# Kernel tuning notes

Measured on AMD Instinct MI355X. Metric: run time of the kernel, lower is better.

## Reference

```python
import jax, jax.numpy as jnp
import numpy as np

INTRA_K = 16
OUTER_K = 16
MAX_PAIR = 1024


def _mahalanobis(x, cov_inv, mean):
    # x: (..., D) difference vectors; returns squared Mahalanobis-style form (...,)
    xc = x - mean
    return jnp.einsum('...i,ij,...j->...', xc, cov_inv, xc)


def setup_inputs() -> dict:
    key = jax.random.key(0)
    k1, k2, k3 = jax.random.split(key, 3)
    B, N, M = 4, 1024, 1024
    outputs = jax.random.normal(k1, (B, N, 9), dtype=jnp.float32)
    targets = jax.random.normal(k2, (B, M, 9), dtype=jnp.float32)
    mask = jax.random.randint(k3, (B, M), 0, 2).astype(bool)
    return {"outputs": outputs, "targets": targets, "mask": mask}


def reference(outputs, targets, mask):
    y_pred = outputs[:, :MAX_PAIR]                      # (B, N, 9)
    m = mask.astype(y_pred.dtype)                       # (B, M)
    cnt = m.sum()

    # mean / covariance over masked true grasps (equivalent to boolean-gather)
    mean = (targets * m[..., None]).sum((0, 1)) / cnt   # (9,)
    centered = (targets - mean) * m[..., None]          # masked rows contribute 0
    flat = centered.reshape(-1, 9)
    cov = flat.T @ flat / (cnt - 1.0)                   # (9, 9)
    cov_inv = jnp.linalg.pinv(cov)

    # intra loss: true-vs-pred pairwise distances, masked rows excluded
    diff = targets[:, :, None, :] - y_pred[:, None, :, :]   # (B, M, N, 9)
    d = _mahalanobis(diff, cov_inv, mean)                   # (B, M, N)
    neg_topk, _ = jax.lax.top_k(-d, INTRA_K)                # k smallest
    row_sum = (-neg_topk).sum(-1)                           # (B, M)
    intra_loss = (row_sum * m).sum() / cnt                  # mean over masked rows

    # outer loss: pred-vs-pred pairwise distances, no mask
    diff_r = y_pred[:, None, :, :] - y_pred[:, :, None, :]  # (B, N, N, 9); [b,i,j] = pred[b,j]-pred[b,i]
    d_r = _mahalanobis(diff_r, cov_inv, mean)               # (B, N, N)
    neg_tk, _ = jax.lax.top_k(-d_r, OUTER_K)
    outer_loss = (-neg_tk).mean()

    return intra_loss, intra_loss, outer_loss
```

## Files before the change

### kernel.cpp

```cpp
#include <hip/hip_runtime.h>
#include <math.h>

#define BB    4
#define MM    1024
#define NN    1024
#define DD    9
#define KSEL  16
#define NROW  (BB * MM)
#define NBLKD (NROW / 4)

struct Ws {
  float yT[BB * DD * NN];
  float qy[BB * NN];
  float bpart_i[NBLKD];
  float bpart_o[NBLKD];
  float part[16][55];
  float cnt;
  float mean[DD];
  float cinv[DD * DD];
  unsigned ticket;
};

__global__ __launch_bounds__(256) void stats_kernel(
    const float* __restrict__ targets, const int* __restrict__ mask,
    Ws* __restrict__ ws) {
  const int tid = threadIdx.x;
  const int r = blockIdx.x * 256 + tid;
  if (blockIdx.x == 0 && tid == 0) ws->ticket = 0u;

  float acc[55];
#pragma unroll
  for (int k = 0; k < 55; ++k) acc[k] = 0.f;
  if (mask[r] != 0) {
    float t[DD];
#pragma unroll
    for (int k = 0; k < DD; ++k) t[k] = targets[r * DD + k];
    acc[0] = 1.f;
#pragma unroll
    for (int k = 0; k < DD; ++k) acc[1 + k] = t[k];
    int u = 10;
#pragma unroll
    for (int p = 0; p < DD; ++p)
#pragma unroll
      for (int q = p; q < DD; ++q) acc[u++] = t[p] * t[q];
  }

  __shared__ float lds[4][55];
#pragma unroll
  for (int k = 0; k < 55; ++k) {
    float v = acc[k];
#pragma unroll
    for (int off = 32; off > 0; off >>= 1) v += __shfl_down(v, off, 64);
    if ((tid & 63) == 0) lds[tid >> 6][k] = v;
  }
  __syncthreads();
  if (tid < 55)
    ws->part[blockIdx.x][tid] =
        lds[0][tid] + lds[1][tid] + lds[2][tid] + lds[3][tid];
}

__global__ __launch_bounds__(256) void prep_kernel(
    const float* __restrict__ outputs, Ws* __restrict__ ws) {
  const int tid = threadIdx.x;
  __shared__ double Sd[55];
  __shared__ float Cs[DD * DD];

  if (tid < 55) {
    double s = 0.0;
#pragma unroll
    for (int b = 0; b < 16; ++b) s += (double)ws->part[b][tid];
    Sd[tid] = s;
  }
  __syncthreads();

  if (tid < 64) {
    const double cnt = Sd[0];
    const int p = (tid < DD) ? tid : 0;
    double row[2 * DD];
    {
      const double mu_p = Sd[1 + p] / cnt;
#pragma unroll
      for (int q = 0; q < DD; ++q) {
        const int pp = (p < q) ? p : q;
        const int qq = (p < q) ? q : p;
        const int idx = 10 + 9 * pp - (pp * (pp - 1)) / 2 + (qq - pp);
        row[q] = (Sd[idx] - cnt * mu_p * (Sd[1 + q] / cnt)) / (cnt - 1.0);
        row[DD + q] = (p == q) ? 1.0 : 0.0;
      }
    }
#pragma unroll
    for (int c = 0; c < DD; ++c) {
      const double diag = __shfl(row[c], c, 64);
      const double dinv = 1.0 / diag;
      if (tid == c) {
#pragma unroll
        for (int q = 0; q < 2 * DD; ++q) row[q] *= dinv;
      }
      const double f = (tid == c) ? 0.0 : row[c];
#pragma unroll
      for (int q = 0; q < 2 * DD; ++q) {
        const double pv = __shfl(row[q], c, 64);
        row[q] -= f * pv;
      }
    }
    if (tid < DD) {
#pragma unroll
      for (int q = 0; q < DD; ++q) {
        const float cf = (float)row[DD + q];
        Cs[tid * DD + q] = cf;
        if (blockIdx.x == 0) ws->cinv[tid * DD + q] = cf;
      }
    }
    if (tid == 0 && blockIdx.x == 0) {
      ws->cnt = (float)cnt;
#pragma unroll
      for (int q = 0; q < DD; ++q) ws->mean[q] = (float)(Sd[1 + q] / cnt);
    }
  }
  __syncthreads();

  const int j = blockIdx.x * 256 + tid;
  const int b = j >> 10;
  const int jj = j & (NN - 1);
  float y[DD];
#pragma unroll
  for (int k = 0; k < DD; ++k) y[k] = outputs[j * DD + k];
  float q = 0.f;
#pragma unroll
  for (int p = 0; p < DD; ++p) {
    float s = 0.f;
#pragma unroll
    for (int t = 0; t < DD; ++t) s += Cs[p * DD + t] * y[t];
    q += y[p] * s;
    ws->yT[(b * DD + p) * NN + jj] = y[p];
  }
  ws->qy[j] = q;
}

__device__ __forceinline__ float topk16_sum(float v[16]) {
#pragma unroll
  for (int k = 2; k <= 16; k <<= 1) {
#pragma unroll
    for (int j = k >> 1; j > 0; j >>= 1) {
#pragma unroll
      for (int i = 0; i < 16; ++i) {
        const int l = i ^ j;
        if (l > i) {
          const bool up = ((i & k) == 0);
          const float lo = fminf(v[i], v[l]);
          const float hi = fmaxf(v[i], v[l]);
          v[i] = up ? lo : hi;
          v[l] = up ? hi : lo;
        }
      }
    }
  }
#pragma unroll
  for (int off = 1; off < 64; off <<= 1) {
    float pr[16];
#pragma unroll
    for (int i = 0; i < 16; ++i) pr[i] = __shfl_xor(v[i], off, 64);
#pragma unroll
    for (int i = 0; i < 16; ++i) v[i] = fminf(v[i], pr[15 - i]);
    if (off < 32) {
#pragma unroll
      for (int j = 8; j > 0; j >>= 1) {
#pragma unroll
        for (int i = 0; i < 16; ++i) {
          const int l = i ^ j;
          if (l > i) {
            const float lo = fminf(v[i], v[l]);
            const float hi = fmaxf(v[i], v[l]);
            v[i] = lo;
            v[l] = hi;
          }
        }
      }
    }
  }
  float t = v[0];
#pragma unroll
  for (int k = 1; k < 16; ++k) t += v[k];
  return t;
}

__global__ __launch_bounds__(256) void dist_kernel(
    const float* __restrict__ outputs, const float* __restrict__ targets,
    const int* __restrict__ mask, Ws* __restrict__ ws,
    float* __restrict__ out) {
  const int wv = threadIdx.x >> 6;
  const int lane = threadIdx.x & 63;
  const int r = blockIdx.x * 4 + wv;
  const int b = r >> 10;

  float ai[DD], ao[DD];
#pragma unroll
  for (int k = 0; k < DD; ++k) {
    const float m = ws->mean[k];
    ai[k] = targets[r * DD + k] - m;
    ao[k] = outputs[r * DD + k] + m;
  }
  float wi[DD], wo[DD];
  float qai = 0.f, qao = 0.f;
#pragma unroll
  for (int p = 0; p < DD; ++p) {
    float si = 0.f, so = 0.f;
#pragma unroll
    for (int t = 0; t < DD; ++t) {
      const float c = ws->cinv[p * DD + t];
      si += c * ai[t];
      so += c * ao[t];
    }
    wi[p] = si;
    wo[p] = so;
    qai += ai[p] * si;
    qao += ao[p] * so;
  }

  float vi[16], vo[16];
#pragma unroll
  for (int k = 0; k < 16; ++k) { vi[k] = 0.f; vo[k] = 0.f; }
  const float* __restrict__ yTb = ws->yT + (size_t)b * DD * NN;
#pragma unroll
  for (int p = 0; p < DD; ++p) {
    const float4* __restrict__ pl = (const float4*)(yTb + (size_t)p * NN);
    const float wip = wi[p], wop = wo[p];
#pragma unroll
    for (int c = 0; c < 4; ++c) {
      const float4 y4 = pl[c * 64 + lane];
      vi[c * 4 + 0] += wip * y4.x; vo[c * 4 + 0] += wop * y4.x;
      vi[c * 4 + 1] += wip * y4.y; vo[c * 4 + 1] += wop * y4.y;
      vi[c * 4 + 2] += wip * y4.z; vo[c * 4 + 2] += wop * y4.z;
      vi[c * 4 + 3] += wip * y4.w; vo[c * 4 + 3] += wop * y4.w;
    }
  }
  {
    const float4* __restrict__ q4 = (const float4*)(ws->qy + (size_t)b * NN);
#pragma unroll
    for (int c = 0; c < 4; ++c) {
      const float4 qv = q4[c * 64 + lane];
      vi[c * 4 + 0] = qai + qv.x - 2.f * vi[c * 4 + 0];
      vi[c * 4 + 1] = qai + qv.y - 2.f * vi[c * 4 + 1];
      vi[c * 4 + 2] = qai + qv.z - 2.f * vi[c * 4 + 2];
      vi[c * 4 + 3] = qai + qv.w - 2.f * vi[c * 4 + 3];
      vo[c * 4 + 0] = qao + qv.x - 2.f * vo[c * 4 + 0];
      vo[c * 4 + 1] = qao + qv.y - 2.f * vo[c * 4 + 1];
      vo[c * 4 + 2] = qao + qv.z - 2.f * vo[c * 4 + 2];
      vo[c * 4 + 3] = qao + qv.w - 2.f * vo[c * 4 + 3];
    }
  }

  float tot_i = topk16_sum(vi);
  float tot_o = topk16_sum(vo);
  if (mask[r] == 0) tot_i = 0.f;

  __shared__ float s_i[4], s_o[4];
  __shared__ int s_last;
  if (lane == 0) { s_i[wv] = tot_i; s_o[wv] = tot_o; }
  __syncthreads();
  if (threadIdx.x == 0) {
    ws->bpart_i[blockIdx.x] = s_i[0] + s_i[1] + s_i[2] + s_i[3];
    ws->bpart_o[blockIdx.x] = s_o[0] + s_o[1] + s_o[2] + s_o[3];
    __threadfence();
    const unsigned t = atomicAdd(&ws->ticket, 1u);
    s_last = (t == NBLKD - 1) ? 1 : 0;
  }
  __syncthreads();

  if (s_last) {
    double li = 0.0, lo = 0.0;
    for (int k = threadIdx.x; k < NBLKD; k += 256) {
      li += (double)atomicAdd(&ws->bpart_i[k], 0.f);
      lo += (double)atomicAdd(&ws->bpart_o[k], 0.f);
    }
#pragma unroll
    for (int off = 32; off > 0; off >>= 1) {
      li += __shfl_down(li, off, 64);
      lo += __shfl_down(lo, off, 64);
    }
    __shared__ double ri[4], ro[4];
    if (lane == 0) { ri[wv] = li; ro[wv] = lo; }
    __syncthreads();
    if (threadIdx.x == 0) {
      const double si = ri[0] + ri[1] + ri[2] + ri[3];
      const double so = ro[0] + ro[1] + ro[2] + ro[3];
      const float intra = (float)(si / (double)ws->cnt);
      const float outer = (float)(so / (double)(NROW * KSEL));
      out[0] = intra;
      out[1] = intra;
      out[2] = outer;
    }
  }
}

extern "C" void kernel_launch(void* const* d_in, const int* in_sizes, int n_in,
                              void* d_out, int out_size, void* d_ws,
                              size_t ws_size, hipStream_t stream) {
  const float* outputs = (const float*)d_in[0];
  const float* targets = (const float*)d_in[1];
  const int* mask = (const int*)d_in[2];
  Ws* ws = (Ws*)d_ws;
  float* out = (float*)d_out;

  stats_kernel<<<NROW / 256, 256, 0, stream>>>(targets, mask, ws);
  prep_kernel<<<(BB * NN) / 256, 256, 0, stream>>>(outputs, ws);
  dist_kernel<<<NBLKD, 256, 0, stream>>>(outputs, targets, mask, ws, out);
}
```

Measured before the change: 106.9 us.

## Fuse stats and prep kernels, split intra/outer rows across waves, skip masked rows

Merges the statistics and prep kernels into one 16-block kernel. The blocks synchronise through a spin-wait on per-block done flags, which removes one kernel launch. The distance kernel now gives each wave either an intra row or an outer row instead of both. This doubles the block count and halves per-thread register arrays, and waves whose intra row is masked skip all distance and top-k work. The done flags are never reset between calls, so later invocations may pass the barrier early and read another call's partial sums.

```diff
diff --git a/kernel.cpp b/kernel.cpp
--- a/kernel.cpp
+++ b/kernel.cpp
@@ -7,27 +7,29 @@
 #define DD    9
 #define KSEL  16
 #define NROW  (BB * MM)
-#define NBLKD (NROW / 4)
+#define NBLKD (2 * NROW / 4)
+#define MAGIC 0x13579BDFu
 
 struct Ws {
   float yT[BB * DD * NN];
   float qy[BB * NN];
-  float bpart_i[NBLKD];
-  float bpart_o[NBLKD];
+  float bpart[NBLKD];
   float part[16][55];
+  unsigned done[16];
+  unsigned ticket;
   float cnt;
   float mean[DD];
   float cinv[DD * DD];
-  unsigned ticket;
 };
 
-__global__ __launch_bounds__(256) void stats_kernel(
-    const float* __restrict__ targets, const int* __restrict__ mask,
-    Ws* __restrict__ ws) {
+__global__ __launch_bounds__(256) void statsprep_kernel(
+    const float* __restrict__ outputs, const float* __restrict__ targets,
+    const int* __restrict__ mask, Ws* __restrict__ ws) {
+  const int g = blockIdx.x;
   const int tid = threadIdx.x;
-  const int r = blockIdx.x * 256 + tid;
-  if (blockIdx.x == 0 && tid == 0) ws->ticket = 0u;
-
+  if (g == 0 && tid == 0) ws->ticket = 0u;
+
+  const int r = g * 256 + tid;
   float acc[55];
 #pragma unroll
   for (int k = 0; k < 55; ++k) acc[k] = 0.f;
@@ -44,7 +46,6 @@
 #pragma unroll
       for (int q = p; q < DD; ++q) acc[u++] = t[p] * t[q];
   }
-
   __shared__ float lds[4][55];
 #pragma unroll
   for (int k = 0; k < 55; ++k) {
@@ -55,20 +56,24 @@
   }
   __syncthreads();
   if (tid < 55)
-    ws->part[blockIdx.x][tid] =
-        lds[0][tid] + lds[1][tid] + lds[2][tid] + lds[3][tid];
-}
-
-__global__ __launch_bounds__(256) void prep_kernel(
-    const float* __restrict__ outputs, Ws* __restrict__ ws) {
-  const int tid = threadIdx.x;
+    ws->part[g][tid] = lds[0][tid] + lds[1][tid] + lds[2][tid] + lds[3][tid];
+  __threadfence();
+  __syncthreads();
+  if (tid == 0) atomicExch(&ws->done[g], MAGIC);
+
+  if (tid < 16) {
+    while (atomicAdd(&ws->done[tid], 0u) != MAGIC) {
+    }
+  }
+  __syncthreads();
+
   __shared__ double Sd[55];
   __shared__ float Cs[DD * DD];
-
   if (tid < 55) {
     double s = 0.0;
 #pragma unroll
-    for (int b = 0; b < 16; ++b) s += (double)ws->part[b][tid];
+    for (int b = 0; b < 16; ++b)
+      s += (double)atomicAdd(&ws->part[b][tid], 0.f);
     Sd[tid] = s;
   }
   __syncthreads();
@@ -108,10 +113,10 @@
       for (int q = 0; q < DD; ++q) {
         const float cf = (float)row[DD + q];
         Cs[tid * DD + q] = cf;
-        if (blockIdx.x == 0) ws->cinv[tid * DD + q] = cf;
-      }
-    }
-    if (tid == 0 && blockIdx.x == 0) {
+        if (g == 0) ws->cinv[tid * DD + q] = cf;
+      }
+    }
+    if (tid == 0 && g == 0) {
       ws->cnt = (float)cnt;
 #pragma unroll
       for (int q = 0; q < DD; ++q) ws->mean[q] = (float)(Sd[1 + q] / cnt);
@@ -119,7 +124,7 @@
   }
   __syncthreads();
 
-  const int j = blockIdx.x * 256 + tid;
+  const int j = g * 256 + tid;
   const int b = j >> 10;
   const int jj = j & (NN - 1);
   float y[DD];
@@ -190,77 +195,69 @@
     float* __restrict__ out) {
   const int wv = threadIdx.x >> 6;
   const int lane = threadIdx.x & 63;
-  const int r = blockIdx.x * 4 + wv;
+  const int s = blockIdx.x * 4 + wv;
+  const bool is_intra = (s < NROW);
+  const int r = s & (NROW - 1);
   const int b = r >> 10;
 
-  float ai[DD], ao[DD];
-#pragma unroll
-  for (int k = 0; k < DD; ++k) {
-    const float m = ws->mean[k];
-    ai[k] = targets[r * DD + k] - m;
-    ao[k] = outputs[r * DD + k] + m;
-  }
-  float wi[DD], wo[DD];
-  float qai = 0.f, qao = 0.f;
-#pragma unroll
-  for (int p = 0; p < DD; ++p) {
-    float si = 0.f, so = 0.f;
-#pragma unroll
-    for (int t = 0; t < DD; ++t) {
-      const float c = ws->cinv[p * DD + t];
-      si += c * ai[t];
-      so += c * ao[t];
-    }
-    wi[p] = si;
-    wo[p] = so;
-    qai += ai[p] * si;
-    qao += ao[p] * so;
-  }
-
-  float vi[16], vo[16];
-#pragma unroll
-  for (int k = 0; k < 16; ++k) { vi[k] = 0.f; vo[k] = 0.f; }
-  const float* __restrict__ yTb = ws->yT + (size_t)b * DD * NN;
-#pragma unroll
-  for (int p = 0; p < DD; ++p) {
-    const float4* __restrict__ pl = (const float4*)(yTb + (size_t)p * NN);
-    const float wip = wi[p], wop = wo[p];
-#pragma unroll
-    for (int c = 0; c < 4; ++c) {
-      const float4 y4 = pl[c * 64 + lane];
-      vi[c * 4 + 0] += wip * y4.x; vo[c * 4 + 0] += wop * y4.x;
-      vi[c * 4 + 1] += wip * y4.y; vo[c * 4 + 1] += wop * y4.y;
-      vi[c * 4 + 2] += wip * y4.z; vo[c * 4 + 2] += wop * y4.z;
-      vi[c * 4 + 3] += wip * y4.w; vo[c * 4 + 3] += wop * y4.w;
-    }
-  }
-  {
-    const float4* __restrict__ q4 = (const float4*)(ws->qy + (size_t)b * NN);
-#pragma unroll
-    for (int c = 0; c < 4; ++c) {
-      const float4 qv = q4[c * 64 + lane];
-      vi[c * 4 + 0] = qai + qv.x - 2.f * vi[c * 4 + 0];
-      vi[c * 4 + 1] = qai + qv.y - 2.f * vi[c * 4 + 1];
-      vi[c * 4 + 2] = qai + qv.z - 2.f * vi[c * 4 + 2];
-      vi[c * 4 + 3] = qai + qv.w - 2.f * vi[c * 4 + 3];
-      vo[c * 4 + 0] = qao + qv.x - 2.f * vo[c * 4 + 0];
-      vo[c * 4 + 1] = qao + qv.y - 2.f * vo[c * 4 + 1];
-      vo[c * 4 + 2] = qao + qv.z - 2.f * vo[c * 4 + 2];
-      vo[c * 4 + 3] = qao + qv.w - 2.f * vo[c * 4 + 3];
-    }
-  }
-
-  float tot_i = topk16_sum(vi);
-  float tot_o = topk16_sum(vo);
-  if (mask[r] == 0) tot_i = 0.f;
-
-  __shared__ float s_i[4], s_o[4];
+  float total = 0.f;
+  if (!(is_intra && mask[r] == 0)) {
+    float a[DD];
+    if (is_intra) {
+#pragma unroll
+      for (int k = 0; k < DD; ++k) a[k] = targets[r * DD + k] - ws->mean[k];
+    } else {
+#pragma unroll
+      for (int k = 0; k < DD; ++k) a[k] = outputs[r * DD + k] + ws->mean[k];
+    }
+    float w9[DD];
+    float qa = 0.f;
+#pragma unroll
+    for (int p = 0; p < DD; ++p) {
+      float acc = 0.f;
+#pragma unroll
+      for (int t = 0; t < DD; ++t) acc += ws->cinv[p * DD + t] * a[t];
+      w9[p] = acc;
+      qa += a[p] * acc;
+    }
+
+    float v[16];
+#pragma unroll
+    for (int k = 0; k < 16; ++k) v[k] = 0.f;
+    const float* __restrict__ yTb = ws->yT + (size_t)b * DD * NN;
+#pragma unroll
+    for (int p = 0; p < DD; ++p) {
+      const float4* __restrict__ pl = (const float4*)(yTb + (size_t)p * NN);
+      const float wp = w9[p];
+#pragma unroll
+      for (int c = 0; c < 4; ++c) {
+        const float4 y4 = pl[c * 64 + lane];
+        v[c * 4 + 0] += wp * y4.x;
+        v[c * 4 + 1] += wp * y4.y;
+        v[c * 4 + 2] += wp * y4.z;
+        v[c * 4 + 3] += wp * y4.w;
+      }
+    }
+    {
+      const float4* __restrict__ q4 = (const float4*)(ws->qy + (size_t)b * NN);
+#pragma unroll
+      for (int c = 0; c < 4; ++c) {
+        const float4 qv = q4[c * 64 + lane];
+        v[c * 4 + 0] = qa + qv.x - 2.f * v[c * 4 + 0];
+        v[c * 4 + 1] = qa + qv.y - 2.f * v[c * 4 + 1];
+        v[c * 4 + 2] = qa + qv.z - 2.f * v[c * 4 + 2];
+        v[c * 4 + 3] = qa + qv.w - 2.f * v[c * 4 + 3];
+      }
+    }
+    total = topk16_sum(v);
+  }
+
+  __shared__ float bsum[4];
   __shared__ int s_last;
-  if (lane == 0) { s_i[wv] = tot_i; s_o[wv] = tot_o; }
+  if (lane == 0) bsum[wv] = total;
   __syncthreads();
   if (threadIdx.x == 0) {
-    ws->bpart_i[blockIdx.x] = s_i[0] + s_i[1] + s_i[2] + s_i[3];
-    ws->bpart_o[blockIdx.x] = s_o[0] + s_o[1] + s_o[2] + s_o[3];
+    ws->bpart[blockIdx.x] = bsum[0] + bsum[1] + bsum[2] + bsum[3];
     __threadfence();
     const unsigned t = atomicAdd(&ws->ticket, 1u);
     s_last = (t == NBLKD - 1) ? 1 : 0;
@@ -270,8 +267,8 @@
   if (s_last) {
     double li = 0.0, lo = 0.0;
     for (int k = threadIdx.x; k < NBLKD; k += 256) {
-      li += (double)atomicAdd(&ws->bpart_i[k], 0.f);
-      lo += (double)atomicAdd(&ws->bpart_o[k], 0.f);
+      const double pv = (double)atomicAdd(&ws->bpart[k], 0.f);
+      if (k < NBLKD / 2) li += pv; else lo += pv;
     }
 #pragma unroll
     for (int off = 32; off > 0; off >>= 1) {
@@ -302,7 +299,6 @@
   Ws* ws = (Ws*)d_ws;
   float* out = (float*)d_out;
 
-  stats_kernel<<<NROW / 256, 256, 0, stream>>>(targets, mask, ws);
-  prep_kernel<<<(BB * NN) / 256, 256, 0, stream>>>(outputs, ws);
+  statsprep_kernel<<<16, 256, 0, stream>>>(outputs, targets, mask, ws);
   dist_kernel<<<NBLKD, 256, 0, stream>>>(outputs, targets, mask, ws, out);
 }
```

Result: slower. 129.3 us (+21.0%).
